# Performance work log

Hardware: AMD Instinct MI355X
Metric: run time of the kernel (lower is better)

Reference implementation:

```python
import jax, jax.numpy as jnp
import numpy as np

VOCAB = 50257
EMB = 128
CTX = 200


def setup_inputs() -> dict:
    key = jax.random.key(0)
    k1, k2, k3, k4, k5 = jax.random.split(key, 5)
    # Forward inputs
    text_onehot = jax.random.normal(k1, (CTX, VOCAB), dtype=jnp.float32)
    length = CTX  # python int scalar
    # Parameters (nn.Linear stores weight as [out, in], bias [out])
    sq = 1.0 / np.sqrt(VOCAB)
    sw = 1.0 / np.sqrt(EMB)
    Wq = jax.random.uniform(k2, (EMB, VOCAB), dtype=jnp.float32, minval=-sq, maxval=sq)
    bq = jax.random.uniform(k3, (EMB,), dtype=jnp.float32, minval=-sq, maxval=sq)
    Ww = jax.random.uniform(k4, (VOCAB, EMB), dtype=jnp.float32, minval=-sw, maxval=sw)
    bw = jax.random.uniform(k5, (VOCAB,), dtype=jnp.float32, minval=-sw, maxval=sw)
    return {"text_onehot": text_onehot, "length": length,
            "Wq": Wq, "bq": bq, "Ww": Ww, "bw": bw}


def reference(text_onehot, length, Wq, bq, Ww, bw):
    # Qembedding: [CTX, VOCAB] @ [VOCAB, EMB] + bias -> [CTX, EMB]
    x = jnp.einsum('tv,ev->te', text_onehot, Wq) + bq
    # dropout is identity in eval mode
    # CBOW mean over context tokens (python loop in original == sum over axis 0)
    hidden = jnp.sum(x, axis=0) / jnp.float32(length)  # [EMB]
    # Wembedding: [EMB] @ [EMB, VOCAB] + bias -> [VOCAB]
    logits = jnp.einsum('e,ve->v', hidden, Ww) + bw
    return jax.nn.log_softmax(logits, axis=-1)
```

## Files before the change

kernel.cpp:

```cpp
#include <hip/hip_runtime.h>
#include <math.h>

#define VOCAB 50257
#define EMB   128
#define CTX   200
#define SLABS 4
#define ROWS_PER_SLAB (CTX / SLABS)
#define NT ((VOCAB + 15) / 16)
#define K3_BLOCKS 786
#define HCHUNKS 32

__global__ void k_colsum(const float* __restrict__ X, float* __restrict__ spart) {
    int v = blockIdx.x * 256 + threadIdx.x;
    if (v >= VOCAB) return;
    const float* p = X + (size_t)(blockIdx.y * ROWS_PER_SLAB) * VOCAB + v;
    float a0 = 0.f, a1 = 0.f, a2 = 0.f, a3 = 0.f, a4 = 0.f;
#pragma unroll
    for (int i = 0; i < ROWS_PER_SLAB / 5; ++i) {
        a0 += p[0 * (size_t)VOCAB];
        a1 += p[1 * (size_t)VOCAB];
        a2 += p[2 * (size_t)VOCAB];
        a3 += p[3 * (size_t)VOCAB];
        a4 += p[4 * (size_t)VOCAB];
        p += 5 * (size_t)VOCAB;
    }
    spart[(size_t)blockIdx.y * VOCAB + v] = ((a0 + a1) + (a2 + a3)) + a4;
}

__global__ void k_hidden(const float* __restrict__ Wq, const float* __restrict__ spart,
                         float* __restrict__ hpart) {
    int e = blockIdx.y;
    const float* row = Wq + (size_t)e * VOCAB;
    float acc = 0.f;
    int stride = gridDim.x * blockDim.x;
    for (int v = blockIdx.x * blockDim.x + threadIdx.x; v < VOCAB; v += stride) {
        float sv = spart[v] + spart[VOCAB + v] + spart[2 * VOCAB + v] + spart[3 * VOCAB + v];
        acc += sv * row[v];
    }
    for (int off = 32; off > 0; off >>= 1) acc += __shfl_down(acc, off, 64);
    __shared__ float wsum[4];
    int lane = threadIdx.x & 63, wid = threadIdx.x >> 6;
    if (lane == 0) wsum[wid] = acc;
    __syncthreads();
    if (threadIdx.x == 0)
        hpart[blockIdx.x * EMB + e] = (wsum[0] + wsum[1]) + (wsum[2] + wsum[3]);
}

__global__ void k_logits(const float* __restrict__ Ww, const float* __restrict__ bw,
                         const float* __restrict__ hpart, const float* __restrict__ bq,
                         const int* __restrict__ lenp,
                         float* __restrict__ logits, float* __restrict__ partials) {
    __shared__ float h[EMB];
    __shared__ float wsum[4];
    if (threadIdx.x < EMB) {
        float len = (float)lenp[0];
        float hr = 0.f;
#pragma unroll
        for (int c = 0; c < HCHUNKS; ++c) hr += hpart[c * EMB + threadIdx.x];
        h[threadIdx.x] = (hr + (float)CTX * bq[threadIdx.x]) / len;
    }
    __syncthreads();

    int group = threadIdx.x >> 4;
    int c     = threadIdx.x & 15;
    float eacc = 0.f;

    for (int tile = blockIdx.x; tile < NT; tile += gridDim.x) {
        int v = tile * 16 + group;
        float acc = 0.f;
        if (v < VOCAB) {
            const float4* row = (const float4*)(Ww + (size_t)v * EMB);
            float4 w0 = row[c * 2];
            float4 w1 = row[c * 2 + 1];
            const float* hp = h + c * 8;
            acc = w0.x * hp[0] + w0.y * hp[1] + w0.z * hp[2] + w0.w * hp[3]
                + w1.x * hp[4] + w1.y * hp[5] + w1.z * hp[6] + w1.w * hp[7];
        }
        acc += __shfl_xor(acc, 1, 64);
        acc += __shfl_xor(acc, 2, 64);
        acc += __shfl_xor(acc, 4, 64);
        acc += __shfl_xor(acc, 8, 64);
        if (v < VOCAB && c == 0) {
            float lg = acc + bw[v];
            logits[v] = lg;
            eacc += expf(lg);
        }
    }

    for (int off = 32; off > 0; off >>= 1) eacc += __shfl_down(eacc, off, 64);
    int lane = threadIdx.x & 63, wid = threadIdx.x >> 6;
    if (lane == 0) wsum[wid] = eacc;
    __syncthreads();
    if (threadIdx.x == 0)
        partials[blockIdx.x] = (wsum[0] + wsum[1]) + (wsum[2] + wsum[3]);
}

__global__ void k_finalize(const float* __restrict__ logits,
                           const float* __restrict__ partials,
                           float* __restrict__ out) {
    __shared__ float wsum[4];
    __shared__ float lz;
    float acc = 0.f;
    for (int i = threadIdx.x; i < K3_BLOCKS; i += 256) acc += partials[i];
    for (int off = 32; off > 0; off >>= 1) acc += __shfl_down(acc, off, 64);
    int lane = threadIdx.x & 63, wid = threadIdx.x >> 6;
    if (lane == 0) wsum[wid] = acc;
    __syncthreads();
    if (threadIdx.x == 0)
        lz = logf((wsum[0] + wsum[1]) + (wsum[2] + wsum[3]));
    __syncthreads();
    int v = blockIdx.x * 256 + threadIdx.x;
    if (v < VOCAB) out[v] = logits[v] - lz;
}

extern "C" void kernel_launch(void* const* d_in, const int* in_sizes, int n_in,
                              void* d_out, int out_size, void* d_ws, size_t ws_size,
                              hipStream_t stream) {
    const float* X    = (const float*)d_in[0];
    const int*   lenp = (const int*)d_in[1];
    const float* Wq   = (const float*)d_in[2];
    const float* bq   = (const float*)d_in[3];
    const float* Ww   = (const float*)d_in[4];
    const float* bw   = (const float*)d_in[5];
    float* out = (float*)d_out;

    float* ws       = (float*)d_ws;
    float* hpart    = ws;
    float* partials = ws + 4096;
    float* spart    = ws + 8192;
    float* logits   = spart;

    dim3 g1((VOCAB + 255) / 256, SLABS);
    k_colsum<<<g1, 256, 0, stream>>>(X, spart);

    dim3 g2(HCHUNKS, EMB);
    k_hidden<<<g2, 256, 0, stream>>>(Wq, spart, hpart);

    k_logits<<<K3_BLOCKS, 256, 0, stream>>>(Ww, bw, hpart, bq, lenp, logits, partials);

    k_finalize<<<(VOCAB + 255) / 256, 256, 0, stream>>>(logits, partials, out);
}
```

Before: 132.7 us.

## Fuse column-sum and hidden projection into one chunked kernel

```diff
diff --git a/kernel.cpp b/kernel.cpp
--- a/kernel.cpp
+++ b/kernel.cpp
@@ -4,68 +4,96 @@
 #define VOCAB 50257
 #define EMB   128
 #define CTX   200
-#define SLABS 4
-#define ROWS_PER_SLAB (CTX / SLABS)
-#define NT ((VOCAB + 15) / 16)
-#define K3_BLOCKS 786
-#define HCHUNKS 32
+#define CHUNK 128
+#define NCHUNK 393
+#define NT    ((VOCAB + 15) / 16)
+#define K3_BLOCKS 394
 
-__global__ void k_colsum(const float* __restrict__ X, float* __restrict__ spart) {
-    int v = blockIdx.x * 256 + threadIdx.x;
-    if (v >= VOCAB) return;
-    const float* p = X + (size_t)(blockIdx.y * ROWS_PER_SLAB) * VOCAB + v;
-    float a0 = 0.f, a1 = 0.f, a2 = 0.f, a3 = 0.f, a4 = 0.f;
-#pragma unroll
-    for (int i = 0; i < ROWS_PER_SLAB / 5; ++i) {
-        a0 += p[0 * (size_t)VOCAB];
-        a1 += p[1 * (size_t)VOCAB];
-        a2 += p[2 * (size_t)VOCAB];
-        a3 += p[3 * (size_t)VOCAB];
-        a4 += p[4 * (size_t)VOCAB];
-        p += 5 * (size_t)VOCAB;
+__global__ __launch_bounds__(128)
+void k12(const float* __restrict__ X, const float* __restrict__ Wq,
+         float* __restrict__ hpart) {
+    __shared__ float svs[CHUNK];
+    __shared__ float hres[EMB];
+    const int b = blockIdx.x, t = threadIdx.x;
+    const int c0 = b * CHUNK;
+    const int v  = c0 + t;
+
+    float sv = 0.f;
+    if (v < VOCAB) {
+        const float* p = X + v;
+        float a0=0.f,a1=0.f,a2=0.f,a3=0.f,a4=0.f,a5=0.f,a6=0.f,a7=0.f,a8=0.f,a9=0.f;
+        for (int i = 0; i < CTX / 10; ++i) {
+            a0 += p[0 * (size_t)VOCAB];
+            a1 += p[1 * (size_t)VOCAB];
+            a2 += p[2 * (size_t)VOCAB];
+            a3 += p[3 * (size_t)VOCAB];
+            a4 += p[4 * (size_t)VOCAB];
+            a5 += p[5 * (size_t)VOCAB];
+            a6 += p[6 * (size_t)VOCAB];
+            a7 += p[7 * (size_t)VOCAB];
+            a8 += p[8 * (size_t)VOCAB];
+            a9 += p[9 * (size_t)VOCAB];
+            p += 10 * (size_t)VOCAB;
+        }
+        sv = (((a0 + a1) + (a2 + a3)) + ((a4 + a5) + (a6 + a7))) + (a8 + a9);
     }
-    spart[(size_t)blockIdx.y * VOCAB + v] = ((a0 + a1) + (a2 + a3)) + a4;
+    svs[t] = sv;
+    __syncthreads();
+
+    const int w = t >> 6, l = t & 63;
+    const float s_lo = svs[l], s_hi = svs[l + 64];
+    const bool full = (c0 + CHUNK <= VOCAB);
+#pragma unroll 4
+    for (int i = 0; i < 64; ++i) {
+        int e = w * 64 + i;
+        const float* row = Wq + (size_t)e * VOCAB + c0;
+        float w0, w1;
+        if (full) { w0 = row[l]; w1 = row[l + 64]; }
+        else {
+            w0 = (c0 + l      < VOCAB) ? row[l]      : 0.f;
+            w1 = (c0 + l + 64 < VOCAB) ? row[l + 64] : 0.f;
+        }
+        float acc = w0 * s_lo + w1 * s_hi;
+        acc += __shfl_xor(acc, 1, 64);
+        acc += __shfl_xor(acc, 2, 64);
+        acc += __shfl_xor(acc, 4, 64);
+        acc += __shfl_xor(acc, 8, 64);
+        acc += __shfl_xor(acc, 16, 64);
+        acc += __shfl_xor(acc, 32, 64);
+        if (l == 0) hres[e] = acc;
+    }
+    __syncthreads();
+    hpart[(size_t)b * EMB + t] = hres[t];
 }
 
-__global__ void k_hidden(const float* __restrict__ Wq, const float* __restrict__ spart,
-                         float* __restrict__ hpart) {
-    int e = blockIdx.y;
-    const float* row = Wq + (size_t)e * VOCAB;
-    float acc = 0.f;
-    int stride = gridDim.x * blockDim.x;
-    for (int v = blockIdx.x * blockDim.x + threadIdx.x; v < VOCAB; v += stride) {
-        float sv = spart[v] + spart[VOCAB + v] + spart[2 * VOCAB + v] + spart[3 * VOCAB + v];
-        acc += sv * row[v];
-    }
-    for (int off = 32; off > 0; off >>= 1) acc += __shfl_down(acc, off, 64);
-    __shared__ float wsum[4];
-    int lane = threadIdx.x & 63, wid = threadIdx.x >> 6;
-    if (lane == 0) wsum[wid] = acc;
-    __syncthreads();
-    if (threadIdx.x == 0)
-        hpart[blockIdx.x * EMB + e] = (wsum[0] + wsum[1]) + (wsum[2] + wsum[3]);
-}
-
-__global__ void k_logits(const float* __restrict__ Ww, const float* __restrict__ bw,
-                         const float* __restrict__ hpart, const float* __restrict__ bq,
-                         const int* __restrict__ lenp,
-                         float* __restrict__ logits, float* __restrict__ partials) {
+__global__ __launch_bounds__(256)
+void k3(const float* __restrict__ Ww, const float* __restrict__ bw,
+        const float* __restrict__ hpart, const float* __restrict__ bq,
+        const int* __restrict__ lenp,
+        float* __restrict__ logits, float* __restrict__ partials) {
     __shared__ float h[EMB];
     __shared__ float wsum[4];
-    if (threadIdx.x < EMB) {
+    const int t = threadIdx.x, b = blockIdx.x;
+    if (t < EMB) {
+        float h0=0.f, h1=0.f, h2=0.f, h3=0.f;
+        int c = 0;
+        for (; c + 4 <= NCHUNK; c += 4) {
+            h0 += hpart[(c + 0) * EMB + t];
+            h1 += hpart[(c + 1) * EMB + t];
+            h2 += hpart[(c + 2) * EMB + t];
+            h3 += hpart[(c + 3) * EMB + t];
+        }
+        for (; c < NCHUNK; ++c) h0 += hpart[c * EMB + t];
+        float hr = (h0 + h1) + (h2 + h3);
         float len = (float)lenp[0];
-        float hr = 0.f;
-#pragma unroll
-        for (int c = 0; c < HCHUNKS; ++c) hr += hpart[c * EMB + threadIdx.x];
-        h[threadIdx.x] = (hr + (float)CTX * bq[threadIdx.x]) / len;
+        h[t] = (hr + (float)CTX * bq[t]) / len;
     }
     __syncthreads();
 
-    int group = threadIdx.x >> 4;
-    int c     = threadIdx.x & 15;
+    int group = t >> 4;
+    int c     = t & 15;
     float eacc = 0.f;
-
-    for (int tile = blockIdx.x; tile < NT; tile += gridDim.x) {
+    for (int tile = b; tile < NT; tile += K3_BLOCKS) {
         int v = tile * 16 + group;
         float acc = 0.f;
         if (v < VOCAB) {
@@ -88,16 +116,16 @@
     }
 
     for (int off = 32; off > 0; off >>= 1) eacc += __shfl_down(eacc, off, 64);
-    int lane = threadIdx.x & 63, wid = threadIdx.x >> 6;
+    int lane = t & 63, wid = t >> 6;
     if (lane == 0) wsum[wid] = eacc;
     __syncthreads();
-    if (threadIdx.x == 0)
-        partials[blockIdx.x] = (wsum[0] + wsum[1]) + (wsum[2] + wsum[3]);
+    if (t == 0)
+        partials[b] = (wsum[0] + wsum[1]) + (wsum[2] + wsum[3]);
 }
 
-__global__ void k_finalize(const float* __restrict__ logits,
-                           const float* __restrict__ partials,
-                           float* __restrict__ out) {
+__global__ __launch_bounds__(256)
+void k4(const float* __restrict__ logits, const float* __restrict__ partials,
+        float* __restrict__ out) {
     __shared__ float wsum[4];
     __shared__ float lz;
     float acc = 0.f;
@@ -126,17 +154,10 @@
 
     float* ws       = (float*)d_ws;
     float* hpart    = ws;
-    float* partials = ws + 4096;
-    float* spart    = ws + 8192;
-    float* logits   = spart;
+    float* partials = ws + NCHUNK * EMB;
+    float* logits   = ws + 51200;
 
-    dim3 g1((VOCAB + 255) / 256, SLABS);
-    k_colsum<<<g1, 256, 0, stream>>>(X, spart);
-
-    dim3 g2(HCHUNKS, EMB);
-    k_hidden<<<g2, 256, 0, stream>>>(Wq, spart, hpart);
-
-    k_logits<<<K3_BLOCKS, 256, 0, stream>>>(Ww, bw, hpart, bq, lenp, logits, partials);
-
-    k_finalize<<<(VOCAB + 255) / 256, 256, 0, stream>>>(logits, partials, out);
+    k12<<<NCHUNK, CHUNK, 0, stream>>>(X, Wq, hpart);
+    k3<<<K3_BLOCKS, 256, 0, stream>>>(Ww, bw, hpart, bq, lenp, logits, partials);
+    k4<<<(VOCAB + 255) / 256, 256, 0, stream>>>(logits, partials, out);
 }
```

Measured after the change: 173.2 us. 30.6% more time.

## Fuse four kernels into one persistent kernel with grid-wide atomic barriers

Applied to the files above, without the earlier changes.

```diff
diff --git a/kernel.cpp b/kernel.cpp
--- a/kernel.cpp
+++ b/kernel.cpp
@@ -4,113 +4,154 @@
 #define VOCAB 50257
 #define EMB   128
 #define CTX   200
-#define SLABS 4
-#define ROWS_PER_SLAB (CTX / SLABS)
+#define CSLABS 197
+#define RSLABS 4
+#define GRID  (CSLABS * RSLABS)
+#define HCHUNKS 32
+#define HTASKS (HCHUNKS * EMB)
 #define NT ((VOCAB + 15) / 16)
-#define K3_BLOCKS 786
-#define HCHUNKS 32
+#define MAGIC 0x5173AB42
+#define SPIN_CAP 80000000u
 
-__global__ void k_colsum(const float* __restrict__ X, float* __restrict__ spart) {
-    int v = blockIdx.x * 256 + threadIdx.x;
-    if (v >= VOCAB) return;
-    const float* p = X + (size_t)(blockIdx.y * ROWS_PER_SLAB) * VOCAB + v;
-    float a0 = 0.f, a1 = 0.f, a2 = 0.f, a3 = 0.f, a4 = 0.f;
-#pragma unroll
-    for (int i = 0; i < ROWS_PER_SLAB / 5; ++i) {
-        a0 += p[0 * (size_t)VOCAB];
-        a1 += p[1 * (size_t)VOCAB];
-        a2 += p[2 * (size_t)VOCAB];
-        a3 += p[3 * (size_t)VOCAB];
-        a4 += p[4 * (size_t)VOCAB];
-        p += 5 * (size_t)VOCAB;
+__device__ __forceinline__ void gbar(int* ready, int* ctr) {
+    __syncthreads();
+    if (threadIdx.x == 0) {
+        unsigned spin = 0;
+        while (__hip_atomic_load(ready, __ATOMIC_ACQUIRE, __HIP_MEMORY_SCOPE_AGENT) != MAGIC
+               && ++spin < SPIN_CAP)
+            __builtin_amdgcn_s_sleep(8);
+        __threadfence();
+        __hip_atomic_fetch_add(ctr, 1, __ATOMIC_ACQ_REL, __HIP_MEMORY_SCOPE_AGENT);
+        spin = 0;
+        while (__hip_atomic_load(ctr, __ATOMIC_ACQUIRE, __HIP_MEMORY_SCOPE_AGENT) < GRID
+               && ++spin < SPIN_CAP)
+            __builtin_amdgcn_s_sleep(8);
     }
-    spart[(size_t)blockIdx.y * VOCAB + v] = ((a0 + a1) + (a2 + a3)) + a4;
+    __syncthreads();
 }
 
-__global__ void k_hidden(const float* __restrict__ Wq, const float* __restrict__ spart,
-                         float* __restrict__ hpart) {
-    int e = blockIdx.y;
-    const float* row = Wq + (size_t)e * VOCAB;
-    float acc = 0.f;
-    int stride = gridDim.x * blockDim.x;
-    for (int v = blockIdx.x * blockDim.x + threadIdx.x; v < VOCAB; v += stride) {
-        float sv = spart[v] + spart[VOCAB + v] + spart[2 * VOCAB + v] + spart[3 * VOCAB + v];
-        acc += sv * row[v];
-    }
-    for (int off = 32; off > 0; off >>= 1) acc += __shfl_down(acc, off, 64);
-    __shared__ float wsum[4];
-    int lane = threadIdx.x & 63, wid = threadIdx.x >> 6;
-    if (lane == 0) wsum[wid] = acc;
-    __syncthreads();
-    if (threadIdx.x == 0)
-        hpart[blockIdx.x * EMB + e] = (wsum[0] + wsum[1]) + (wsum[2] + wsum[3]);
-}
-
-__global__ void k_logits(const float* __restrict__ Ww, const float* __restrict__ bw,
-                         const float* __restrict__ hpart, const float* __restrict__ bq,
-                         const int* __restrict__ lenp,
-                         float* __restrict__ logits, float* __restrict__ partials) {
+__global__ __launch_bounds__(256, 4)
+void k_fused(const float* __restrict__ X, const int* __restrict__ lenp,
+             const float* __restrict__ Wq, const float* __restrict__ bq,
+             const float* __restrict__ Ww, const float* __restrict__ bw,
+             float* __restrict__ out,
+             float* __restrict__ spart,
+             float* __restrict__ hpart,
+             float* __restrict__ partials,
+             int*   __restrict__ bar) {
+    const int b = blockIdx.x, t = threadIdx.x;
     __shared__ float h[EMB];
     __shared__ float wsum[4];
-    if (threadIdx.x < EMB) {
+    __shared__ float lzs;
+    float* logits = spart;
+
+    if (b == 0 && t == 0) {
+        __hip_atomic_store(&bar[16], 0, __ATOMIC_RELAXED, __HIP_MEMORY_SCOPE_AGENT);
+        __hip_atomic_store(&bar[32], 0, __ATOMIC_RELAXED, __HIP_MEMORY_SCOPE_AGENT);
+        __hip_atomic_store(&bar[48], 0, __ATOMIC_RELAXED, __HIP_MEMORY_SCOPE_AGENT);
+        __hip_atomic_store(&bar[0], MAGIC, __ATOMIC_RELEASE, __HIP_MEMORY_SCOPE_AGENT);
+    }
+
+    {
+        int c = b % CSLABS, r = b / CSLABS;
+        int v = c * 256 + t;
+        if (v < VOCAB) {
+            const float* p = X + (size_t)(r * 50) * VOCAB + v;
+            float a0=0.f,a1=0.f,a2=0.f,a3=0.f,a4=0.f,a5=0.f,a6=0.f,a7=0.f,a8=0.f,a9=0.f;
+            for (int i = 0; i < 5; ++i) {
+                a0 += p[0 * (size_t)VOCAB];
+                a1 += p[1 * (size_t)VOCAB];
+                a2 += p[2 * (size_t)VOCAB];
+                a3 += p[3 * (size_t)VOCAB];
+                a4 += p[4 * (size_t)VOCAB];
+                a5 += p[5 * (size_t)VOCAB];
+                a6 += p[6 * (size_t)VOCAB];
+                a7 += p[7 * (size_t)VOCAB];
+                a8 += p[8 * (size_t)VOCAB];
+                a9 += p[9 * (size_t)VOCAB];
+                p += 10 * (size_t)VOCAB;
+            }
+            spart[(size_t)(b / CSLABS) * VOCAB + v] =
+                (((a0 + a1) + (a2 + a3)) + ((a4 + a5) + (a6 + a7))) + (a8 + a9);
+        }
+    }
+    gbar(bar, bar + 16);
+
+    for (int task = b; task < HTASKS; task += GRID) {
+        int chunk = task & (HCHUNKS - 1), e = task >> 5;
+        const float* row = Wq + (size_t)e * VOCAB;
+        float acc = 0.f;
+        for (int v = chunk * 256 + t; v < VOCAB; v += HCHUNKS * 256) {
+            float sv = spart[v] + spart[VOCAB + v]
+                     + spart[2 * VOCAB + v] + spart[3 * VOCAB + v];
+            acc += sv * row[v];
+        }
+        for (int off = 32; off > 0; off >>= 1) acc += __shfl_down(acc, off, 64);
+        int lane = t & 63, wid = t >> 6;
+        if (lane == 0) wsum[wid] = acc;
+        __syncthreads();
+        if (t == 0)
+            hpart[chunk * EMB + e] = (wsum[0] + wsum[1]) + (wsum[2] + wsum[3]);
+        __syncthreads();
+    }
+    gbar(bar, bar + 32);
+
+    if (t < EMB) {
         float len = (float)lenp[0];
         float hr = 0.f;
 #pragma unroll
-        for (int c = 0; c < HCHUNKS; ++c) hr += hpart[c * EMB + threadIdx.x];
-        h[threadIdx.x] = (hr + (float)CTX * bq[threadIdx.x]) / len;
+        for (int c = 0; c < HCHUNKS; ++c) hr += hpart[c * EMB + t];
+        h[t] = (hr + (float)CTX * bq[t]) / len;
     }
     __syncthreads();
+    {
+        int group = t >> 4;
+        int c     = t & 15;
+        float eacc = 0.f;
+        for (int tile = b; tile < NT; tile += GRID) {
+            int v = tile * 16 + group;
+            float acc = 0.f;
+            if (v < VOCAB) {
+                const float4* row = (const float4*)(Ww + (size_t)v * EMB);
+                float4 w0 = row[c * 2];
+                float4 w1 = row[c * 2 + 1];
+                const float* hp = h + c * 8;
+                acc = w0.x * hp[0] + w0.y * hp[1] + w0.z * hp[2] + w0.w * hp[3]
+                    + w1.x * hp[4] + w1.y * hp[5] + w1.z * hp[6] + w1.w * hp[7];
+            }
+            acc += __shfl_xor(acc, 1, 64);
+            acc += __shfl_xor(acc, 2, 64);
+            acc += __shfl_xor(acc, 4, 64);
+            acc += __shfl_xor(acc, 8, 64);
+            if (v < VOCAB && c == 0) {
+                float lg = acc + bw[v];
+                logits[v] = lg;
+                eacc += expf(lg);
+            }
+        }
+        for (int off = 32; off > 0; off >>= 1) eacc += __shfl_down(eacc, off, 64);
+        int lane = t & 63, wid = t >> 6;
+        if (lane == 0) wsum[wid] = eacc;
+        __syncthreads();
+        if (t == 0)
+            partials[b] = (wsum[0] + wsum[1]) + (wsum[2] + wsum[3]);
+    }
+    gbar(bar, bar + 48);
 
-    int group = threadIdx.x >> 4;
-    int c     = threadIdx.x & 15;
-    float eacc = 0.f;
-
-    for (int tile = blockIdx.x; tile < NT; tile += gridDim.x) {
-        int v = tile * 16 + group;
+    if (b >= (VOCAB + 255) / 256) return;
+    {
         float acc = 0.f;
-        if (v < VOCAB) {
-            const float4* row = (const float4*)(Ww + (size_t)v * EMB);
-            float4 w0 = row[c * 2];
-            float4 w1 = row[c * 2 + 1];
-            const float* hp = h + c * 8;
-            acc = w0.x * hp[0] + w0.y * hp[1] + w0.z * hp[2] + w0.w * hp[3]
-                + w1.x * hp[4] + w1.y * hp[5] + w1.z * hp[6] + w1.w * hp[7];
-        }
-        acc += __shfl_xor(acc, 1, 64);
-        acc += __shfl_xor(acc, 2, 64);
-        acc += __shfl_xor(acc, 4, 64);
-        acc += __shfl_xor(acc, 8, 64);
-        if (v < VOCAB && c == 0) {
-            float lg = acc + bw[v];
-            logits[v] = lg;
-            eacc += expf(lg);
-        }
+        for (int i = t; i < GRID; i += 256) acc += partials[i];
+        for (int off = 32; off > 0; off >>= 1) acc += __shfl_down(acc, off, 64);
+        int lane = t & 63, wid = t >> 6;
+        if (lane == 0) wsum[wid] = acc;
+        __syncthreads();
+        if (t == 0)
+            lzs = logf((wsum[0] + wsum[1]) + (wsum[2] + wsum[3]));
+        __syncthreads();
+        int v = b * 256 + t;
+        if (v < VOCAB) out[v] = logits[v] - lzs;
     }
-
-    for (int off = 32; off > 0; off >>= 1) eacc += __shfl_down(eacc, off, 64);
-    int lane = threadIdx.x & 63, wid = threadIdx.x >> 6;
-    if (lane == 0) wsum[wid] = eacc;
-    __syncthreads();
-    if (threadIdx.x == 0)
-        partials[blockIdx.x] = (wsum[0] + wsum[1]) + (wsum[2] + wsum[3]);
-}
-
-__global__ void k_finalize(const float* __restrict__ logits,
-                           const float* __restrict__ partials,
-                           float* __restrict__ out) {
-    __shared__ float wsum[4];
-    __shared__ float lz;
-    float acc = 0.f;
-    for (int i = threadIdx.x; i < K3_BLOCKS; i += 256) acc += partials[i];
-    for (int off = 32; off > 0; off >>= 1) acc += __shfl_down(acc, off, 64);
-    int lane = threadIdx.x & 63, wid = threadIdx.x >> 6;
-    if (lane == 0) wsum[wid] = acc;
-    __syncthreads();
-    if (threadIdx.x == 0)
-        lz = logf((wsum[0] + wsum[1]) + (wsum[2] + wsum[3]));
-    __syncthreads();
-    int v = blockIdx.x * 256 + threadIdx.x;
-    if (v < VOCAB) out[v] = logits[v] - lz;
 }
 
 extern "C" void kernel_launch(void* const* d_in, const int* in_sizes, int n_in,
@@ -127,16 +168,9 @@
     float* ws       = (float*)d_ws;
     float* hpart    = ws;
     float* partials = ws + 4096;
+    int*   bar      = (int*)(ws + 5120);
     float* spart    = ws + 8192;
-    float* logits   = spart;
 
-    dim3 g1((VOCAB + 255) / 256, SLABS);
-    k_colsum<<<g1, 256, 0, stream>>>(X, spart);
-
-    dim3 g2(HCHUNKS, EMB);
-    k_hidden<<<g2, 256, 0, stream>>>(Wq, spart, hpart);
-
-    k_logits<<<K3_BLOCKS, 256, 0, stream>>>(Ww, bw, hpart, bq, lenp, logits, partials);
-
-    k_finalize<<<(VOCAB + 255) / 256, 256, 0, stream>>>(logits, partials, out);
+    k_fused<<<GRID, 256, 0, stream>>>(X, lenp, Wq, bq, Ww, bw, out,
+                                      spart, hpart, partials, bar);
 }
```

New measurement: 403.4 us. 204% more time.

## Fuse finalize into logits via last-block atomic, widen colsum slabs, batch hidden rows

Applied to the files above, without the earlier changes.

```diff
diff --git a/kernel.cpp b/kernel.cpp
--- a/kernel.cpp
+++ b/kernel.cpp
@@ -4,68 +4,92 @@
 #define VOCAB 50257
 #define EMB   128
 #define CTX   200
-#define SLABS 4
-#define ROWS_PER_SLAB (CTX / SLABS)
+#define CSLABS 197
+#define RSLABS 8
+#define ROWS   25
+#define HCHUNKS 32
+#define K3_BLOCKS 788
 #define NT ((VOCAB + 15) / 16)
-#define K3_BLOCKS 786
-#define HCHUNKS 32
 
-__global__ void k_colsum(const float* __restrict__ X, float* __restrict__ spart) {
+__global__ __launch_bounds__(256)
+void k1(const float* __restrict__ X, float* __restrict__ spart,
+        int* __restrict__ done) {
+    if (blockIdx.x == 0 && blockIdx.y == 0 && threadIdx.x == 0)
+        __hip_atomic_store(done, 0, __ATOMIC_RELAXED, __HIP_MEMORY_SCOPE_AGENT);
     int v = blockIdx.x * 256 + threadIdx.x;
     if (v >= VOCAB) return;
-    const float* p = X + (size_t)(blockIdx.y * ROWS_PER_SLAB) * VOCAB + v;
-    float a0 = 0.f, a1 = 0.f, a2 = 0.f, a3 = 0.f, a4 = 0.f;
+    const float* p = X + (size_t)(blockIdx.y * ROWS) * VOCAB + v;
+    float a[ROWS];
 #pragma unroll
-    for (int i = 0; i < ROWS_PER_SLAB / 5; ++i) {
-        a0 += p[0 * (size_t)VOCAB];
-        a1 += p[1 * (size_t)VOCAB];
-        a2 += p[2 * (size_t)VOCAB];
-        a3 += p[3 * (size_t)VOCAB];
-        a4 += p[4 * (size_t)VOCAB];
-        p += 5 * (size_t)VOCAB;
-    }
-    spart[(size_t)blockIdx.y * VOCAB + v] = ((a0 + a1) + (a2 + a3)) + a4;
+    for (int j = 0; j < ROWS; ++j) a[j] = p[(size_t)j * VOCAB];
+    float s0 = ((a[0] + a[1]) + (a[2] + a[3])) + a[4];
+    float s1 = ((a[5] + a[6]) + (a[7] + a[8])) + a[9];
+    float s2 = ((a[10] + a[11]) + (a[12] + a[13])) + a[14];
+    float s3 = ((a[15] + a[16]) + (a[17] + a[18])) + a[19];
+    float s4 = ((a[20] + a[21]) + (a[22] + a[23])) + a[24];
+    spart[(size_t)blockIdx.y * VOCAB + v] = ((s0 + s1) + (s2 + s3)) + s4;
 }
 
-__global__ void k_hidden(const float* __restrict__ Wq, const float* __restrict__ spart,
-                         float* __restrict__ hpart) {
-    int e = blockIdx.y;
-    const float* row = Wq + (size_t)e * VOCAB;
-    float acc = 0.f;
-    int stride = gridDim.x * blockDim.x;
-    for (int v = blockIdx.x * blockDim.x + threadIdx.x; v < VOCAB; v += stride) {
-        float sv = spart[v] + spart[VOCAB + v] + spart[2 * VOCAB + v] + spart[3 * VOCAB + v];
-        acc += sv * row[v];
+__global__ __launch_bounds__(256)
+void k2(const float* __restrict__ Wq, const float* __restrict__ spart,
+        float* __restrict__ hpart) {
+    const int chunk = blockIdx.x;
+    const int e0    = blockIdx.y * 4;
+    const int t     = threadIdx.x;
+    const float* r0 = Wq + (size_t)(e0 + 0) * VOCAB;
+    const float* r1 = Wq + (size_t)(e0 + 1) * VOCAB;
+    const float* r2 = Wq + (size_t)(e0 + 2) * VOCAB;
+    const float* r3 = Wq + (size_t)(e0 + 3) * VOCAB;
+    float a0 = 0.f, a1 = 0.f, a2 = 0.f, a3 = 0.f;
+    for (int v = chunk * 256 + t; v < VOCAB; v += HCHUNKS * 256) {
+        float sv = 0.f;
+#pragma unroll
+        for (int s = 0; s < RSLABS; ++s) sv += spart[(size_t)s * VOCAB + v];
+        a0 += sv * r0[v];
+        a1 += sv * r1[v];
+        a2 += sv * r2[v];
+        a3 += sv * r3[v];
     }
-    for (int off = 32; off > 0; off >>= 1) acc += __shfl_down(acc, off, 64);
-    __shared__ float wsum[4];
-    int lane = threadIdx.x & 63, wid = threadIdx.x >> 6;
-    if (lane == 0) wsum[wid] = acc;
+    for (int off = 32; off > 0; off >>= 1) {
+        a0 += __shfl_down(a0, off, 64);
+        a1 += __shfl_down(a1, off, 64);
+        a2 += __shfl_down(a2, off, 64);
+        a3 += __shfl_down(a3, off, 64);
+    }
+    __shared__ float wsum[4][4];
+    int lane = t & 63, wid = t >> 6;
+    if (lane == 0) { wsum[wid][0] = a0; wsum[wid][1] = a1;
+                     wsum[wid][2] = a2; wsum[wid][3] = a3; }
     __syncthreads();
-    if (threadIdx.x == 0)
-        hpart[blockIdx.x * EMB + e] = (wsum[0] + wsum[1]) + (wsum[2] + wsum[3]);
+    if (t < 4)
+        hpart[chunk * EMB + e0 + t] =
+            (wsum[0][t] + wsum[1][t]) + (wsum[2][t] + wsum[3][t]);
 }
 
-__global__ void k_logits(const float* __restrict__ Ww, const float* __restrict__ bw,
-                         const float* __restrict__ hpart, const float* __restrict__ bq,
-                         const int* __restrict__ lenp,
-                         float* __restrict__ logits, float* __restrict__ partials) {
+__global__ __launch_bounds__(256)
+void k3(const float* __restrict__ Ww, const float* __restrict__ bw,
+        const float* __restrict__ hpart, const float* __restrict__ bq,
+        const int* __restrict__ lenp,
+        float* __restrict__ logits, float* __restrict__ partials,
+        int* __restrict__ done, float* __restrict__ out) {
     __shared__ float h[EMB];
     __shared__ float wsum[4];
-    if (threadIdx.x < EMB) {
-        float len = (float)lenp[0];
+    __shared__ int lastFlag;
+    __shared__ float lzs;
+    const int t = threadIdx.x, b = blockIdx.x;
+
+    if (t < EMB) {
         float hr = 0.f;
 #pragma unroll
-        for (int c = 0; c < HCHUNKS; ++c) hr += hpart[c * EMB + threadIdx.x];
-        h[threadIdx.x] = (hr + (float)CTX * bq[threadIdx.x]) / len;
+        for (int c = 0; c < HCHUNKS; ++c) hr += hpart[c * EMB + t];
+        h[t] = (hr + (float)CTX * bq[t]) / (float)lenp[0];
     }
     __syncthreads();
 
-    int group = threadIdx.x >> 4;
-    int c     = threadIdx.x & 15;
+    int group = t >> 4;
+    int c     = t & 15;
     float eacc = 0.f;
-
-    for (int tile = blockIdx.x; tile < NT; tile += gridDim.x) {
+    for (int tile = b; tile < NT; tile += K3_BLOCKS) {
         int v = tile * 16 + group;
         float acc = 0.f;
         if (v < VOCAB) {
@@ -86,31 +110,32 @@
             eacc += expf(lg);
         }
     }
-
     for (int off = 32; off > 0; off >>= 1) eacc += __shfl_down(eacc, off, 64);
-    int lane = threadIdx.x & 63, wid = threadIdx.x >> 6;
+    int lane = t & 63, wid = t >> 6;
     if (lane == 0) wsum[wid] = eacc;
     __syncthreads();
-    if (threadIdx.x == 0)
-        partials[blockIdx.x] = (wsum[0] + wsum[1]) + (wsum[2] + wsum[3]);
-}
+    if (t == 0) {
+        partials[b] = (wsum[0] + wsum[1]) + (wsum[2] + wsum[3]);
+        __threadfence();
+        int old = __hip_atomic_fetch_add(done, 1, __ATOMIC_ACQ_REL,
+                                         __HIP_MEMORY_SCOPE_AGENT);
+        lastFlag = (old == K3_BLOCKS - 1);
+    }
+    __syncthreads();
+    if (!lastFlag) return;
 
-__global__ void k_finalize(const float* __restrict__ logits,
-                           const float* __restrict__ partials,
-                           float* __restrict__ out) {
-    __shared__ float wsum[4];
-    __shared__ float lz;
+    __threadfence();
     float acc = 0.f;
-    for (int i = threadIdx.x; i < K3_BLOCKS; i += 256) acc += partials[i];
+    for (int i = t; i < K3_BLOCKS; i += 256) acc += partials[i];
     for (int off = 32; off > 0; off >>= 1) acc += __shfl_down(acc, off, 64);
-    int lane = threadIdx.x & 63, wid = threadIdx.x >> 6;
     if (lane == 0) wsum[wid] = acc;
     __syncthreads();
-    if (threadIdx.x == 0)
-        lz = logf((wsum[0] + wsum[1]) + (wsum[2] + wsum[3]));
+    if (t == 0)
+        lzs = logf((wsum[0] + wsum[1]) + (wsum[2] + wsum[3]));
     __syncthreads();
-    int v = blockIdx.x * 256 + threadIdx.x;
-    if (v < VOCAB) out[v] = logits[v] - lz;
+    float lz = lzs;
+#pragma unroll 4
+    for (int v = t; v < VOCAB; v += 256) out[v] = logits[v] - lz;
 }
 
 extern "C" void kernel_launch(void* const* d_in, const int* in_sizes, int n_in,
@@ -127,16 +152,16 @@
     float* ws       = (float*)d_ws;
     float* hpart    = ws;
     float* partials = ws + 4096;
+    int*   done     = (int*)(ws + 5120);
     float* spart    = ws + 8192;
     float* logits   = spart;
 
-    dim3 g1((VOCAB + 255) / 256, SLABS);
-    k_colsum<<<g1, 256, 0, stream>>>(X, spart);
+    dim3 g1(CSLABS, RSLABS);
+    k1<<<g1, 256, 0, stream>>>(X, spart, done);
 
-    dim3 g2(HCHUNKS, EMB);
-    k_hidden<<<g2, 256, 0, stream>>>(Wq, spart, hpart);
+    dim3 g2(HCHUNKS, EMB / 4);
+    k2<<<g2, 256, 0, stream>>>(Wq, spart, hpart);
 
-    k_logits<<<K3_BLOCKS, 256, 0, stream>>>(Ww, bw, hpart, bq, lenp, logits, partials);
-
-    k_finalize<<<(VOCAB + 255) / 256, 256, 0, stream>>>(logits, partials, out);
+    k3<<<K3_BLOCKS, 256, 0, stream>>>(Ww, bw, hpart, bq, lenp,
+                                      logits, partials, done, out);
 }
```

After: 166.6 us. +25.5%, slower.
